# Kernel optimization log

Measured on AMD Instinct MI355X. Metric: run time of the kernel, lower is better.

Reference implementation:

```python
import jax, jax.numpy as jnp
import numpy as np
from jax import lax

B, T, V, LAT, U, P = 256, 128, 42, 200, 512, 3  # batch, seq, vocab, latent, lstm units, num_prop


def setup_inputs() -> dict:
    key = jax.random.key(0)
    ks = jax.random.split(key, 40)
    g = lambda i, shape, s=0.05: (jax.random.normal(ks[i], shape, jnp.float32) * s)
    inp = {
        'X': jax.random.randint(ks[0], (B, T), 0, V, jnp.int64 if jax.config.jax_enable_x64 else jnp.int32),
        'Y': jax.random.randint(ks[1], (B, T), 0, V, jnp.int32),
        'C': jax.random.normal(ks[2], (B, P), jnp.float32),
        'L': jax.random.randint(ks[3], (B,), 1, T + 1, jnp.int32),
        'eps': jax.random.normal(ks[4], (B, LAT), jnp.float32),
        'emb_enc': g(5, (V, LAT), 0.1),
        'emb_dec': g(6, (V, LAT), 0.1),
        # encoder stacked LSTM: layer0 input dim = LAT + P, layers 1-2 input dim = U
        'enc_k0': g(7, (LAT + P, 4 * U)), 'enc_rk0': g(8, (U, 4 * U)), 'enc_b0': jnp.zeros((4 * U,), jnp.float32),
        'enc_k1': g(9, (U, 4 * U)), 'enc_rk1': g(10, (U, 4 * U)), 'enc_b1': jnp.zeros((4 * U,), jnp.float32),
        'enc_k2': g(11, (U, 4 * U)), 'enc_rk2': g(12, (U, 4 * U)), 'enc_b2': jnp.zeros((4 * U,), jnp.float32),
        # decoder stacked LSTM: layer0 input dim = 2*LAT + P
        'dec_k0': g(13, (2 * LAT + P, 4 * U)), 'dec_rk0': g(14, (U, 4 * U)), 'dec_b0': jnp.zeros((4 * U,), jnp.float32),
        'dec_k1': g(15, (U, 4 * U)), 'dec_rk1': g(16, (U, 4 * U)), 'dec_b1': jnp.zeros((4 * U,), jnp.float32),
        'dec_k2': g(17, (U, 4 * U)), 'dec_rk2': g(18, (U, 4 * U)), 'dec_b2': jnp.zeros((4 * U,), jnp.float32),
        'Wm': g(19, (U, LAT)), 'bm': jnp.zeros((LAT,), jnp.float32),
        'Ws': g(20, (U, LAT)), 'bs': jnp.zeros((LAT,), jnp.float32),
        'Wo': g(21, (U, V)), 'bo': jnp.zeros((V,), jnp.float32),
    }
    return inp


def _lstm_step(x, h, c, k, rk, b):
    # Keras LSTMCell gate order: i, f, g(candidate), o
    z = x @ k + h @ rk + b
    i, f, gg, o = jnp.split(z, 4, axis=-1)
    c2 = jax.nn.sigmoid(f) * c + jax.nn.sigmoid(i) * jnp.tanh(gg)
    h2 = jax.nn.sigmoid(o) * jnp.tanh(c2)
    return h2, c2


def _run_stacked(inp, params):
    # inp: [B, T, D]; params: list of 3 (kernel, recurrent_kernel, bias)
    b = inp.shape[0]
    init = tuple((jnp.zeros((b, U), inp.dtype), jnp.zeros((b, U), inp.dtype)) for _ in range(3))

    def scan_fn(carry, x_t):
        h_in = x_t
        new = []
        for (h, c), (k, rk, bb) in zip(carry, params):
            h2, c2 = _lstm_step(h_in, h, c, k, rk, bb)
            new.append((h2, c2))
            h_in = h2
        return tuple(new), h_in

    carry, ys = lax.scan(scan_fn, init, jnp.swapaxes(inp, 0, 1))
    return jnp.swapaxes(ys, 0, 1), carry  # [B,T,U], final states


def reference(X, Y, C, L, eps, emb_enc, emb_dec,
              enc_k0, enc_rk0, enc_b0, enc_k1, enc_rk1, enc_b1, enc_k2, enc_rk2, enc_b2,
              dec_k0, dec_rk0, dec_b0, dec_k1, dec_rk1, dec_b1, dec_k2, dec_rk2, dec_b2,
              Wm, bm, Ws, bs, Wo, bo):
    enc_params = [(enc_k0, enc_rk0, enc_b0), (enc_k1, enc_rk1, enc_b1), (enc_k2, enc_rk2, enc_b2)]
    dec_params = [(dec_k0, dec_rk0, dec_b0), (dec_k1, dec_rk1, dec_b1), (dec_k2, dec_rk2, dec_b2)]

    # ---- encode ----
    Xe = emb_enc[X]                                       # [B,T,LAT]
    Ct = jnp.broadcast_to(C[:, None, :], (B, T, P))
    enc_in = jnp.concatenate([Xe, Ct], axis=-1)           # [B,T,LAT+P]
    _, enc_states = _run_stacked(enc_in, enc_params)
    h = enc_states[-1][1]                                 # CELL state of last layer (state[-1][1])
    mean = h @ Wm + bm
    log_sigma = h @ Ws + bs
    z = mean + jnp.exp(log_sigma / 2.0) * eps             # [B,LAT]

    # ---- decode ----
    Zt = jnp.broadcast_to(z[:, None, :], (B, T, LAT))
    Xd = emb_dec[X]
    dec_in = jnp.concatenate([Zt, Xd, Ct], axis=-1)       # [B,T,2*LAT+P]
    dec_out, _ = _run_stacked(dec_in, dec_params)
    pre = dec_out @ Wo + bo                               # pre-softmax logits [B,T,V]

    # ---- losses ----
    logp = jax.nn.log_softmax(pre, axis=-1)
    ce = -jnp.take_along_axis(logp, Y[..., None].astype(jnp.int32), axis=-1)[..., 0]  # [B,T]
    weights = (jnp.arange(T)[None, :] < L[:, None]).astype(jnp.float32)
    recon = jnp.mean(ce * weights)
    latent = -0.5 * jnp.mean(1.0 + log_sigma - jnp.square(mean) - jnp.exp(log_sigma))
    loss = recon + latent
    return loss, recon, latent
```

## Files before the change

### kernel.cpp

```cpp
#include <hip/hip_runtime.h>

#define B_ 256
#define T_ 128
#define V_ 42
#define LAT_ 200
#define U_ 512
#define G4_ 2048
#define NBLK 196
#define FI(r, m) ((((r) * 2) + (m)) * 32)
#define SLOT_ ((size_t)B_ * U_)
#define LS_ ((size_t)129 * SLOT_)

typedef unsigned short ushort_t;
typedef __attribute__((ext_vector_type(8))) short bf8;
typedef __attribute__((ext_vector_type(4))) float f4;

__device__ __forceinline__ ushort_t f2bf(float f) {
  union { float f; unsigned int i; } v; v.f = f;
  unsigned int r = v.i + 0x7fffu + ((v.i >> 16) & 1u);
  return (ushort_t)(r >> 16);
}
__device__ __forceinline__ float sigf(float x) { return 1.f / (1.f + __expf(-x)); }
__device__ __forceinline__ float tanhfast(float x) {
  float e = __expf(2.f * x);
  return 1.f - 2.f / (e + 1.f);
}
__device__ __forceinline__ void wait_vm0() {
  asm volatile("s_waitcnt vmcnt(0)" ::: "memory");
}
__device__ __forceinline__ void st_wt_b16(void* p, ushort_t v) {
  unsigned int vv = v;
  asm volatile("global_store_short %0, %1, off sc0 sc1" :: "v"(p), "v"(vv) : "memory");
}
__device__ __forceinline__ void st_wt_b32(void* p, unsigned int v) {
  asm volatile("global_store_dword %0, %1, off sc0 sc1" :: "v"(p), "v"(v) : "memory");
}

__global__ __launch_bounds__(256) void table_kernel(const float* emb, const float* k0, int roff, float* table) {
  int v = blockIdx.x, tid = threadIdx.x;
  __shared__ float e[LAT_];
  for (int i = tid; i < LAT_; i += 256) e[i] = emb[v * LAT_ + i];
  __syncthreads();
  for (int j = tid; j < G4_; j += 256) {
    float s = 0.f;
    for (int n = 0; n < LAT_; n++) s += e[n] * k0[(size_t)(roff + n) * G4_ + j];
    table[v * G4_ + j] = s;
  }
}

__device__ __forceinline__ size_t mat_off_u4(int m) {
  if (m == 0) return 0;
  if (m == 1) return 147456;
  if (m < 10) return 360448 + (size_t)(m - 2) * 131072;
  return 1409024;
}

struct SwzSrc {
  const float *enc_rk0, *enc_k0, *enc_b0;
  const float *dec_rk0, *dec_k0, *dec_b0;
  const float *tabE, *tabD;
  const float *encK1, *encR1, *encK2, *encR2;
  const float *decK1, *decR1, *decK2, *decR2;
  const float *Wo;
  ushort_t* dst;
};

__device__ float swz_val(const SwzSrc& s, int mat, int k, int n) {
  switch (mat) {
    case 0: {
      if (k < 512) return s.enc_rk0[(size_t)k * G4_ + n];
      int i = k - 512;
      if (i < 42) return s.tabE[(size_t)i * G4_ + n];
      if (i < 45) return s.enc_k0[(size_t)(200 + i - 42) * G4_ + n];
      if (i == 45) return s.enc_b0[n];
      return 0.f;
    }
    case 1: {
      if (k < 512) return s.dec_rk0[(size_t)k * G4_ + n];
      int i = k - 512;
      if (i < 200) return s.dec_k0[(size_t)i * G4_ + n];
      if (i < 256) return 0.f;
      i -= 256;
      if (i < 42) return s.tabD[(size_t)i * G4_ + n];
      if (i < 45) return s.dec_k0[(size_t)(400 + i - 42) * G4_ + n];
      if (i == 45) return s.dec_b0[n];
      return 0.f;
    }
    case 2: return s.encK1[(size_t)k * G4_ + n];
    case 3: return s.encR1[(size_t)k * G4_ + n];
    case 4: return s.encK2[(size_t)k * G4_ + n];
    case 5: return s.encR2[(size_t)k * G4_ + n];
    case 6: return s.decK1[(size_t)k * G4_ + n];
    case 7: return s.decR1[(size_t)k * G4_ + n];
    case 8: return s.decK2[(size_t)k * G4_ + n];
    case 9: return s.decR2[(size_t)k * G4_ + n];
    default: return (n < V_) ? s.Wo[(size_t)k * V_ + n] : 0.f;
  }
}

__global__ __launch_bounds__(256) void swz_ext_kernel(SwzSrc s) {
  int b = blockIdx.x, tid = threadIdx.x;
  int mat, nt16;
  if (b < 1280) { mat = b >> 7; nt16 = b & 127; } else { mat = 10; nt16 = b - 1280; }
  int ktMax = (mat == 0) ? 18 : (mat == 1) ? 26 : 16;
  int lane = tid & 63, l15 = lane & 15, q = lane >> 4;
  int n = nt16 * 16 + l15;
  uint4* dst = (uint4*)s.dst;
  size_t off = mat_off_u4(mat);
  for (int kt = tid >> 6; kt < ktMax; kt += 4) {
    ushort_t o[8];
    int kb = kt * 32 + q * 8;
#pragma unroll
    for (int j = 0; j < 8; j++) o[j] = f2bf(swz_val(s, mat, kb + j, n));
    dst[off + ((size_t)nt16 * ktMax + kt) * 64 + lane] = *(const uint4*)o;
  }
}

struct PP {
  const ushort_t* swz;
  ushort_t* ring;
  float* c2g; ushort_t* zf16; float* sums; int* bar; int* gen; int* flg; float* out;
  const float *enc_b1, *enc_b2, *dec_b1, *dec_b2;
  const float *Wm, *bm, *Ws, *bs, *eps, *C, *bo;
  const int *X, *Y, *Lb;
};

__device__ __forceinline__ void grid_barrier(int* bar, int* gen) {
  __builtin_amdgcn_fence(__ATOMIC_RELEASE, "agent");
  __syncthreads();
  if (threadIdx.x == 0) {
    int g = __hip_atomic_load(gen, __ATOMIC_RELAXED, __HIP_MEMORY_SCOPE_AGENT);
    if (__hip_atomic_fetch_add(bar, 1, __ATOMIC_ACQ_REL, __HIP_MEMORY_SCOPE_AGENT) == NBLK - 1) {
      __hip_atomic_store(bar, 0, __ATOMIC_RELAXED, __HIP_MEMORY_SCOPE_AGENT);
      __hip_atomic_store(gen, g + 1, __ATOMIC_RELEASE, __HIP_MEMORY_SCOPE_AGENT);
    } else {
      int gg;
      do {
        __builtin_amdgcn_s_sleep(8);
        gg = __hip_atomic_load(gen, __ATOMIC_ACQUIRE, __HIP_MEMORY_SCOPE_AGENT);
      } while (gg == g);
    }
  }
  __syncthreads();
  __builtin_amdgcn_fence(__ATOMIC_ACQUIRE, "agent");
}

__device__ __forceinline__ void wait_flags(const int* f, int cnt, int target) {
  int lane = threadIdx.x & 63;
  bool need = (lane * 2) < cnt;
  const unsigned long long* a = (const unsigned long long*)f + (need ? lane : 0);
  for (;;) {
    unsigned long long v = __hip_atomic_load(a, __ATOMIC_RELAXED, __HIP_MEMORY_SCOPE_AGENT);
    bool bad = need && ((int)v < target || (int)(v >> 32) < target);
    if (__ballot(bad) == 0ull) return;
    __builtin_amdgcn_s_sleep(8);
  }
}

#define MFMA(a, bfrag, c) __builtin_amdgcn_mfma_f32_16x16x32_bf16((a), (bfrag), (c), 0, 0, 0)

__global__ __launch_bounds__(256, 1) void persist(PP p) {
  __shared__ uint4 wlds4[8192];
  const int b = blockIdx.x, tid = threadIdx.x;
  const int lane = tid & 63, w = tid >> 6, q = lane >> 4, l15 = lane & 15;
  const int role = b < 64 ? 0 : b < 128 ? 1 : b < 192 ? 2 : 3;
  const int idx = b & 63;
  const int ut = idx >> 1;
  const int mi = idx & 1;
  const int m0 = mi * 128;
  const int rw = m0 + w * 32;
  const int u = ut * 16 + l15;
  const uint4* swzU4 = (const uint4*)p.swz;
  const int cb = b - 192;

  unsigned char* tok = (unsigned char*)wlds4 + 106496;
  unsigned char* ytok = (unsigned char*)wlds4 + 49152;

  ushort_t cb0[2][3];
  if (role == 0) {
#pragma unroll
    for (int ms = 0; ms < 2; ms++)
#pragma unroll
      for (int j = 0; j < 3; j++) cb0[ms][j] = f2bf(p.C[(rw + ms * 16 + l15) * 3 + j]);
  }

  const int pubidx = FI(role, mi) + ut;

  float ce_local = 0.f;
  float boR0 = 0.f, boR1 = 0.f, boR2 = 0.f;
  int Lr[4] = {0, 0, 0, 0};
  int pub = 0;

  for (int phase = 0; phase < 2; phase++) {
    const bool dec = (phase == 1);

    if (dec) {
      grid_barrier(p.bar, p.gen);
      if (b < 50) {
        int lat0 = b * 4;
        int row = tid;
        float m[4], ls[4];
#pragma unroll
        for (int lc = 0; lc < 4; lc++) { m[lc] = p.bm[lat0 + lc]; ls[lc] = p.bs[lat0 + lc]; }
        const float* cr = p.c2g + (size_t)row * U_;
        for (int k = 0; k < U_; k++) {
          float hv = cr[k];
#pragma unroll
          for (int lc = 0; lc < 4; lc++) {
            m[lc] += hv * p.Wm[k * LAT_ + lat0 + lc];
            ls[lc] += hv * p.Ws[k * LAT_ + lat0 + lc];
          }
        }
        float kl = 0.f;
#pragma unroll
        for (int lc = 0; lc < 4; lc++) {
          int lat = lat0 + lc;
          float zz = m[lc] + __expf(0.5f * ls[lc]) * p.eps[row * LAT_ + lat];
          p.zf16[row * 256 + lat] = f2bf(zz);
          kl += 1.f + ls[lc] - m[lc] * m[lc] - __expf(ls[lc]);
        }
        float* red = (float*)wlds4;
        red[tid] = kl; __syncthreads();
        for (int st = 128; st > 0; st >>= 1) { if (tid < st) red[tid] += red[tid + st]; __syncthreads(); }
        if (tid == 0) atomicAdd(p.sums + 1, red[0]);
      }
      __syncthreads();
    }

    if (role == 0) {
      if (!dec) {
        size_t mo = mat_off_u4(0);
        for (int g = 0; g < 4; g++) {
          int nt16 = g * 32 + ut;
          size_t src = mo + (size_t)nt16 * 18 * 64;
          int dst = g * 18 * 64;
          for (int i = tid; i < 18 * 64; i += 256) wlds4[dst + i] = swzU4[src + i];
        }
        for (int i = tid; i < 128 * T_; i += 256) {
          int r = i >> 7, t = i & 127;
          tok[r * 133 + t] = (unsigned char)p.X[(size_t)(m0 + r) * T_ + t];
        }
      } else {
        size_t mo = mat_off_u4(1);
        for (int g = 0; g < 4; g++) {
          int nt16 = g * 32 + ut;
          size_t src = mo + (size_t)nt16 * 26 * 64;
          int dst = g * 18 * 64;
          for (int i = tid; i < 16 * 64; i += 256) wlds4[dst + i] = swzU4[src + i];
          for (int i = tid; i < 2 * 64; i += 256) wlds4[dst + 16 * 64 + i] = swzU4[src + 24 * 64 + i];
          for (int i = tid; i < 8 * 64; i += 256) wlds4[4608 + g * 512 + i] = swzU4[src + 16 * 64 + i];
        }
      }
    } else if (role <= 2) {
      int matK = dec ? (role == 1 ? 6 : 8) : (role == 1 ? 2 : 4);
      for (int gm = 0; gm < 2; gm++) {
        size_t mo = mat_off_u4(matK + gm);
        for (int g = 0; g < 4; g++) {
          int nt16 = g * 32 + ut;
          size_t src = mo + (size_t)nt16 * 1024;
          int dst = gm * 4096 + g * 1024;
          for (int i = tid; i < 1024; i += 256) wlds4[dst + i] = swzU4[src + i];
        }
      }
    } else if (dec) {
      size_t mo = mat_off_u4(10);
      for (int i = tid; i < 3072; i += 256) wlds4[i] = swzU4[mo + i];
      for (int i = tid; i < 64 * T_; i += 256) {
        int r = i >> 7, t = i & 127;
        ytok[r * 133 + t] = (unsigned char)p.Y[(size_t)(cb * 64 + r) * T_ + t];
      }
      int r0c = cb * 64 + w * 16;
      boR0 = p.bo[l15]; boR1 = p.bo[16 + l15]; boR2 = (l15 < 10) ? p.bo[32 + l15] : 0.f;
#pragma unroll
      for (int r = 0; r < 4; r++) Lr[r] = p.Lb[r0c + q * 4 + r];
    }
    __syncthreads();

    float creg[2][4];
#pragma unroll
    for (int ms = 0; ms < 2; ms++)
#pragma unroll
      for (int r = 0; r < 4; r++) creg[ms][r] = 0.f;
    float bias[4] = {0.f, 0.f, 0.f, 0.f};
    if (role == 1 || role == 2) {
      const float* bb = dec ? (role == 1 ? p.dec_b1 : p.dec_b2) : (role == 1 ? p.enc_b1 : p.enc_b2);
#pragma unroll
      for (int g = 0; g < 4; g++) bias[g] = bb[g * 512 + u];
    }

    const int* myp = nullptr; int myc = 0;
    if (role == 0) {
      if (w == 0) { myp = p.flg + FI(0, mi); myc = 32; }
    } else if (role == 1) {
      if (w == 0) { myp = p.flg + FI(0, mi); myc = 32; }
      else if (w == 1) { myp = p.flg + FI(1, mi); myc = 32; }
    } else if (role == 2) {
      if (w == 0) { myp = p.flg + FI(1, mi); myc = 32; }
      else if (w == 1) { myp = p.flg + FI(2, mi); myc = 32; }
    } else {
      if (w == 0 && dec) { myp = p.flg + FI(2, cb >> 1); myc = 32; }
    }

    grid_barrier(p.bar, p.gen);

    f4 zacc[2][4];
#pragma unroll
    for (int ms = 0; ms < 2; ms++)
#pragma unroll
      for (int g = 0; g < 4; g++) zacc[ms][g] = (f4){0.f, 0.f, 0.f, 0.f};
    if (role == 0 && dec) {
      const ushort_t* Az0 = p.zf16 + (rw + l15) * 256 + q * 8;
#pragma unroll
      for (int kz = 0; kz < 8; kz++) {
        bf8 a0 = *(const bf8*)(Az0 + kz * 32);
        bf8 a1 = *(const bf8*)(Az0 + 16 * 256 + kz * 32);
#pragma unroll
        for (int g = 0; g < 4; g++) {
          bf8 bbf = *(const bf8*)&wlds4[4608 + g * 512 + kz * 64 + lane];
          zacc[0][g] = MFMA(a0, bbf, zacc[0][g]);
          zacc[1][g] = MFMA(a1, bbf, zacc[1][g]);
        }
      }
    }

    const int smax = dec ? T_ + 3 : T_ + 2;
    for (int s = 0; s < smax; s++) {
      pub++;
      if (myc) wait_flags(myp, myc, pub - 1);
      __syncthreads();

      const int lag = (role <= 2) ? role : 3;
      const int t = s - lag;
      if (role == 3) {
        if (dec && t >= 0 && t < T_) {
          int r0c = cb * 64 + w * 16;
          const ushort_t* Ar = p.ring + 2 * LS_ + (size_t)(t + 1) * SLOT_ + (size_t)(r0c + l15) * U_ + q * 8;
          f4 a3[3];
#pragma unroll
          for (int nt = 0; nt < 3; nt++) a3[nt] = (f4){0.f, 0.f, 0.f, 0.f};
#pragma unroll 4
          for (int kt = 0; kt < 16; kt++) {
            bf8 a = *(const bf8*)(Ar + kt * 32);
#pragma unroll
            for (int nt = 0; nt < 3; nt++) {
              bf8 bbf = *(const bf8*)&wlds4[nt * 1024 + kt * 64 + lane];
              a3[nt] = MFMA(a, bbf, a3[nt]);
            }
          }
#pragma unroll
          for (int r = 0; r < 4; r++) {
            float v0 = a3[0][r] + boR0;
            float v1 = a3[1][r] + boR1;
            float v2 = (l15 < 10) ? a3[2][r] + boR2 : -3.0e38f;
            float mx = fmaxf(fmaxf(v0, v1), v2);
            mx = fmaxf(mx, __shfl_xor(mx, 1)); mx = fmaxf(mx, __shfl_xor(mx, 2));
            mx = fmaxf(mx, __shfl_xor(mx, 4)); mx = fmaxf(mx, __shfl_xor(mx, 8));
            float se = __expf(v0 - mx) + __expf(v1 - mx) + ((l15 < 10) ? __expf(v2 - mx) : 0.f);
            int yv = ytok[(w * 16 + q * 4 + r) * 133 + t];
            float py = (l15 == yv ? v0 : 0.f) + (l15 + 16 == yv ? v1 : 0.f) + (l15 + 32 == yv ? v2 : 0.f);
            se += __shfl_xor(se, 1); se += __shfl_xor(se, 2); se += __shfl_xor(se, 4); se += __shfl_xor(se, 8);
            py += __shfl_xor(py, 1); py += __shfl_xor(py, 2); py += __shfl_xor(py, 4); py += __shfl_xor(py, 8);
            if (l15 == 0 && t < Lr[r]) ce_local += mx + __logf(se) - py;
          }
        }
      } else if (t >= 0 && t < T_) {
        f4 acc[2][4];
#pragma unroll
        for (int ms = 0; ms < 2; ms++)
#pragma unroll
          for (int g = 0; g < 4; g++) acc[ms][g] = zacc[ms][g];

        const ushort_t* hin = p.ring + (size_t)role * LS_ + (size_t)t * SLOT_;
        ushort_t* hout = p.ring + (size_t)role * LS_ + (size_t)(t + 1) * SLOT_;
        const ushort_t* Ah0 = hin + (size_t)(rw + l15) * U_ + q * 8;
        const ushort_t* Ah1 = Ah0 + 16 * U_;

        if (role == 0) {
          const int KT64 = 18 * 64;
#pragma unroll 4
          for (int kt = 0; kt < 16; kt++) {
            bf8 a0 = *(const bf8*)(Ah0 + kt * 32);
            bf8 a1 = *(const bf8*)(Ah1 + kt * 32);
#pragma unroll
            for (int g = 0; g < 4; g++) {
              bf8 bbf = *(const bf8*)&wlds4[g * KT64 + kt * 64 + lane];
              acc[0][g] = MFMA(a0, bbf, acc[0][g]);
              acc[1][g] = MFMA(a1, bbf, acc[1][g]);
            }
          }
          int xv0 = tok[(w * 32 + l15) * 133 + t];
          int xv1 = tok[(w * 32 + 16 + l15) * 133 + t];
#pragma unroll
          for (int ktc = 0; ktc < 2; ktc++) {
            union { ushort_t us[8]; bf8 v; } a0u, a1u;
#pragma unroll
            for (int j = 0; j < 8; j++) {
              int id = ktc * 32 + q * 8 + j;
              ushort_t v0 = (id == xv0) ? (ushort_t)0x3F80 : (ushort_t)0;
              ushort_t v1 = (id == xv1) ? (ushort_t)0x3F80 : (ushort_t)0;
              if (id >= 42 && id < 45) { v0 = cb0[0][id - 42]; v1 = cb0[1][id - 42]; }
              if (id == 45) { v0 = 0x3F80; v1 = 0x3F80; }
              a0u.us[j] = v0; a1u.us[j] = v1;
            }
            int kt = 16 + ktc;
#pragma unroll
            for (int g = 0; g < 4; g++) {
              bf8 bbf = *(const bf8*)&wlds4[g * KT64 + kt * 64 + lane];
              acc[0][g] = MFMA(a0u.v, bbf, acc[0][g]);
              acc[1][g] = MFMA(a1u.v, bbf, acc[1][g]);
            }
          }
        } else {
          const ushort_t* xin = p.ring + (size_t)(role - 1) * LS_ + (size_t)(t + 1) * SLOT_;
          const ushort_t* Ax0 = xin + (size_t)(rw + l15) * U_ + q * 8;
          const ushort_t* Ax1 = Ax0 + 16 * U_;
#pragma unroll 4
          for (int kt = 0; kt < 16; kt++) {
            bf8 a0 = *(const bf8*)(Ax0 + kt * 32);
            bf8 a1 = *(const bf8*)(Ax1 + kt * 32);
#pragma unroll
            for (int g = 0; g < 4; g++) {
              bf8 bbf = *(const bf8*)&wlds4[g * 1024 + kt * 64 + lane];
              acc[0][g] = MFMA(a0, bbf, acc[0][g]);
              acc[1][g] = MFMA(a1, bbf, acc[1][g]);
            }
          }
#pragma unroll 4
          for (int kt = 0; kt < 16; kt++) {
            bf8 a0 = *(const bf8*)(Ah0 + kt * 32);
            bf8 a1 = *(const bf8*)(Ah1 + kt * 32);
#pragma unroll
            for (int g = 0; g < 4; g++) {
              bf8 bbf = *(const bf8*)&wlds4[4096 + g * 1024 + kt * 64 + lane];
              acc[0][g] = MFMA(a0, bbf, acc[0][g]);
              acc[1][g] = MFMA(a1, bbf, acc[1][g]);
            }
          }
        }

#pragma unroll
        for (int ms = 0; ms < 2; ms++)
#pragma unroll
          for (int r = 0; r < 4; r++) {
            int row = rw + ms * 16 + q * 4 + r;
            float zi = acc[ms][0][r] + bias[0];
            float zf = acc[ms][1][r] + bias[1];
            float zg = acc[ms][2][r] + bias[2];
            float zo = acc[ms][3][r] + bias[3];
            float cp = creg[ms][r];
            float cn = sigf(zf) * cp + sigf(zi) * tanhfast(zg);
            float hn = sigf(zo) * tanhfast(cn);
            creg[ms][r] = cn;
            st_wt_b16(&hout[(size_t)row * U_ + u], f2bf(hn));
            if (!dec && role == 2 && t == T_ - 1) p.c2g[(size_t)row * U_ + u] = cn;
          }
      }
      wait_vm0();
      __syncthreads();
      if (tid == 0 && role < 3) st_wt_b32(p.flg + pubidx, (unsigned int)pub);
    }
  }

  if (role == 3 && l15 == 0) atomicAdd(p.sums + 0, ce_local);
  grid_barrier(p.bar, p.gen);
  if (b == 0 && tid == 0) {
    float recon = p.sums[0] * (1.f / ((float)B_ * (float)T_));
    float latent = -0.5f * p.sums[1] * (1.f / ((float)B_ * (float)LAT_));
    p.out[0] = recon + latent;
    p.out[1] = recon;
    p.out[2] = latent;
  }
}

extern "C" void kernel_launch(void* const* d_in, const int* in_sizes, int n_in,
                              void* d_out, int out_size, void* d_ws, size_t ws_size,
                              hipStream_t stream) {
  const int*   X       = (const int*)d_in[0];
  const int*   Y       = (const int*)d_in[1];
  const float* C       = (const float*)d_in[2];
  const int*   L       = (const int*)d_in[3];
  const float* eps     = (const float*)d_in[4];
  const float* emb_enc = (const float*)d_in[5];
  const float* emb_dec = (const float*)d_in[6];
  const float* enc_k0  = (const float*)d_in[7];
  const float* enc_rk0 = (const float*)d_in[8];
  const float* enc_b0  = (const float*)d_in[9];
  const float* enc_k1  = (const float*)d_in[10];
  const float* enc_rk1 = (const float*)d_in[11];
  const float* enc_b1  = (const float*)d_in[12];
  const float* enc_k2  = (const float*)d_in[13];
  const float* enc_rk2 = (const float*)d_in[14];
  const float* enc_b2  = (const float*)d_in[15];
  const float* dec_k0  = (const float*)d_in[16];
  const float* dec_rk0 = (const float*)d_in[17];
  const float* dec_b0  = (const float*)d_in[18];
  const float* dec_k1  = (const float*)d_in[19];
  const float* dec_rk1 = (const float*)d_in[20];
  const float* dec_b1  = (const float*)d_in[21];
  const float* dec_k2  = (const float*)d_in[22];
  const float* dec_rk2 = (const float*)d_in[23];
  const float* dec_b2  = (const float*)d_in[24];
  const float* Wm      = (const float*)d_in[25];
  const float* bm      = (const float*)d_in[26];
  const float* Ws      = (const float*)d_in[27];
  const float* bs      = (const float*)d_in[28];
  const float* Wo      = (const float*)d_in[29];
  const float* bo      = (const float*)d_in[30];
  float* out = (float*)d_out;
  (void)in_sizes; (void)n_in; (void)out_size; (void)ws_size;

  char* wsb = (char*)d_ws;
  size_t o = 0;
  auto take = [&](size_t bytes) -> char* { char* p = wsb + o; o += (bytes + 255) & ~(size_t)255; return p; };

  float* c2g  = (float*)take((size_t)B_ * U_ * 4);
  ushort_t* zf16 = (ushort_t*)take((size_t)B_ * 256 * 2);
  float* sums = (float*)take(8);
  int* bar = (int*)take(4);
  int* gen = (int*)take(4);
  int* flg = (int*)take(4 * 2 * 32 * 4);
  size_t zero_bytes = o;
  ushort_t* ring = (ushort_t*)take(3 * LS_ * 2);
  ushort_t* swz = (ushort_t*)take((size_t)1412096 * 16);
  float* tabE = (float*)take((size_t)V_ * G4_ * 4);
  float* tabD = (float*)take((size_t)V_ * G4_ * 4);

  hipMemsetAsync(wsb, 0, zero_bytes, stream);
  for (int l = 0; l < 3; l++)
    hipMemsetAsync(ring + (size_t)l * LS_, 0, SLOT_ * 2, stream);

  table_kernel<<<V_, 256, 0, stream>>>(emb_enc, enc_k0, 0, tabE);
  table_kernel<<<V_, 256, 0, stream>>>(emb_dec, dec_k0, 200, tabD);

  SwzSrc ss;
  ss.enc_rk0 = enc_rk0; ss.enc_k0 = enc_k0; ss.enc_b0 = enc_b0;
  ss.dec_rk0 = dec_rk0; ss.dec_k0 = dec_k0; ss.dec_b0 = dec_b0;
  ss.tabE = tabE; ss.tabD = tabD;
  ss.encK1 = enc_k1; ss.encR1 = enc_rk1; ss.encK2 = enc_k2; ss.encR2 = enc_rk2;
  ss.decK1 = dec_k1; ss.decR1 = dec_rk1; ss.decK2 = dec_k2; ss.decR2 = dec_rk2;
  ss.Wo = Wo; ss.dst = swz;
  swz_ext_kernel<<<1283, 256, 0, stream>>>(ss);

  PP pp;
  pp.swz = swz; pp.ring = ring;
  pp.c2g = c2g; pp.zf16 = zf16; pp.sums = sums; pp.bar = bar; pp.gen = gen; pp.flg = flg; pp.out = out;
  pp.enc_b1 = enc_b1; pp.enc_b2 = enc_b2; pp.dec_b1 = dec_b1; pp.dec_b2 = dec_b2;
  pp.Wm = Wm; pp.bm = bm; pp.Ws = Ws; pp.bs = bs; pp.eps = eps; pp.C = C; pp.bo = bo;
  pp.X = X; pp.Y = Y; pp.Lb = L;
  persist<<<NBLK, 256, 0, stream>>>(pp);
}
```

Baseline: 5.388 ms.

## Interleave block roles across XCDs, grow grid to 256, and tighten spin-waits

Block roles are now assigned by blockIdx modulo 8, so each LSTM layer/half and the output blocks are spread across XCDs. The grid grows to 256 blocks, and the extra blocks act as helpers that only do the latent projection and skip the recurrent loop. The grid barrier sleeps less between polls, and the flag wait polls one int per lane with no sleep, to cut wake-up latency on each per-step handoff. The h-state store now does a plain store followed by a write-through store, which adds a redundant write, and the busier polling adds memory traffic.

```diff
diff --git a/kernel.cpp b/kernel.cpp
--- a/kernel.cpp
+++ b/kernel.cpp
@@ -6,7 +6,7 @@
 #define LAT_ 200
 #define U_ 512
 #define G4_ 2048
-#define NBLK 196
+#define NBLK 256
 #define FI(r, m) ((((r) * 2) + (m)) * 32)
 #define SLOT_ ((size_t)B_ * U_)
 #define LS_ ((size_t)129 * SLOT_)
@@ -136,7 +136,7 @@
     } else {
       int gg;
       do {
-        __builtin_amdgcn_s_sleep(8);
+        __builtin_amdgcn_s_sleep(1);
         gg = __hip_atomic_load(gen, __ATOMIC_ACQUIRE, __HIP_MEMORY_SCOPE_AGENT);
       } while (gg == g);
     }
@@ -147,14 +147,12 @@
 
 __device__ __forceinline__ void wait_flags(const int* f, int cnt, int target) {
   int lane = threadIdx.x & 63;
-  bool need = (lane * 2) < cnt;
-  const unsigned long long* a = (const unsigned long long*)f + (need ? lane : 0);
-  for (;;) {
-    unsigned long long v = __hip_atomic_load(a, __ATOMIC_RELAXED, __HIP_MEMORY_SCOPE_AGENT);
-    bool bad = need && ((int)v < target || (int)(v >> 32) < target);
-    if (__ballot(bad) == 0ull) return;
-    __builtin_amdgcn_s_sleep(8);
-  }
+  const int* a = f + (lane < cnt ? lane : 0);
+  bool bad;
+  do {
+    int v = __hip_atomic_load(a, __ATOMIC_RELAXED, __HIP_MEMORY_SCOPE_AGENT);
+    bad = (lane < cnt) && (v < target);
+  } while (__ballot(bad) != 0ull);
 }
 
 #define MFMA(a, bfrag, c) __builtin_amdgcn_mfma_f32_16x16x32_bf16((a), (bfrag), (c), 0, 0, 0)
@@ -163,15 +161,17 @@
   __shared__ uint4 wlds4[8192];
   const int b = blockIdx.x, tid = threadIdx.x;
   const int lane = tid & 63, w = tid >> 6, q = lane >> 4, l15 = lane & 15;
-  const int role = b < 64 ? 0 : b < 128 ? 1 : b < 192 ? 2 : 3;
-  const int idx = b & 63;
-  const int ut = idx >> 1;
-  const int mi = idx & 1;
+
+  const int grp = b & 7, rank = b >> 3;
+  int role, mi = 0, cb = 0, pid = -1;
+  if (grp < 6) { role = grp >> 1; mi = grp & 1; }
+  else if (grp == 6 && rank < 4) { role = 3; cb = rank; mi = rank >> 1; }
+  else { role = 4; pid = (grp == 6) ? rank - 4 : 28 + rank; }
+  const int ut = rank;
   const int m0 = mi * 128;
   const int rw = m0 + w * 32;
   const int u = ut * 16 + l15;
   const uint4* swzU4 = (const uint4*)p.swz;
-  const int cb = b - 192;
 
   unsigned char* tok = (unsigned char*)wlds4 + 106496;
   unsigned char* ytok = (unsigned char*)wlds4 + 49152;
@@ -196,8 +196,8 @@
 
     if (dec) {
       grid_barrier(p.bar, p.gen);
-      if (b < 50) {
-        int lat0 = b * 4;
+      if (pid >= 0 && pid < 50) {
+        int lat0 = pid * 4;
         int row = tid;
         float m[4], ls[4];
 #pragma unroll
@@ -262,7 +262,7 @@
           for (int i = tid; i < 1024; i += 256) wlds4[dst + i] = swzU4[src + i];
         }
       }
-    } else if (dec) {
+    } else if (role == 3 && dec) {
       size_t mo = mat_off_u4(10);
       for (int i = tid; i < 3072; i += 256) wlds4[i] = swzU4[mo + i];
       for (int i = tid; i < 64 * T_; i += 256) {
@@ -297,7 +297,7 @@
     } else if (role == 2) {
       if (w == 0) { myp = p.flg + FI(1, mi); myc = 32; }
       else if (w == 1) { myp = p.flg + FI(2, mi); myc = 32; }
-    } else {
+    } else if (role == 3) {
       if (w == 0 && dec) { myp = p.flg + FI(2, cb >> 1); myc = 32; }
     }
 
@@ -323,141 +323,146 @@
       }
     }
 
-    const int smax = dec ? T_ + 3 : T_ + 2;
-    for (int s = 0; s < smax; s++) {
-      pub++;
-      if (myc) wait_flags(myp, myc, pub - 1);
-      __syncthreads();
-
-      const int lag = (role <= 2) ? role : 3;
-      const int t = s - lag;
-      if (role == 3) {
-        if (dec && t >= 0 && t < T_) {
-          int r0c = cb * 64 + w * 16;
-          const ushort_t* Ar = p.ring + 2 * LS_ + (size_t)(t + 1) * SLOT_ + (size_t)(r0c + l15) * U_ + q * 8;
-          f4 a3[3];
-#pragma unroll
-          for (int nt = 0; nt < 3; nt++) a3[nt] = (f4){0.f, 0.f, 0.f, 0.f};
+    if (role <= 3) {
+      const int smax = dec ? T_ + 3 : T_ + 2;
+      for (int s = 0; s < smax; s++) {
+        pub++;
+        if (myc) wait_flags(myp, myc, pub - 1);
+        __syncthreads();
+
+        const int lag = (role <= 2) ? role : 3;
+        const int t = s - lag;
+        if (role == 3) {
+          if (dec && t >= 0 && t < T_) {
+            int r0c = cb * 64 + w * 16;
+            const ushort_t* Ar = p.ring + 2 * LS_ + (size_t)(t + 1) * SLOT_ + (size_t)(r0c + l15) * U_ + q * 8;
+            f4 a3[3];
+#pragma unroll
+            for (int nt = 0; nt < 3; nt++) a3[nt] = (f4){0.f, 0.f, 0.f, 0.f};
 #pragma unroll 4
-          for (int kt = 0; kt < 16; kt++) {
-            bf8 a = *(const bf8*)(Ar + kt * 32);
-#pragma unroll
-            for (int nt = 0; nt < 3; nt++) {
-              bf8 bbf = *(const bf8*)&wlds4[nt * 1024 + kt * 64 + lane];
-              a3[nt] = MFMA(a, bbf, a3[nt]);
+            for (int kt = 0; kt < 16; kt++) {
+              bf8 a = *(const bf8*)(Ar + kt * 32);
+#pragma unroll
+              for (int nt = 0; nt < 3; nt++) {
+                bf8 bbf = *(const bf8*)&wlds4[nt * 1024 + kt * 64 + lane];
+                a3[nt] = MFMA(a, bbf, a3[nt]);
+              }
+            }
+#pragma unroll
+            for (int r = 0; r < 4; r++) {
+              float v0 = a3[0][r] + boR0;
+              float v1 = a3[1][r] + boR1;
+              float v2 = (l15 < 10) ? a3[2][r] + boR2 : -3.0e38f;
+              float mx = fmaxf(fmaxf(v0, v1), v2);
+              mx = fmaxf(mx, __shfl_xor(mx, 1)); mx = fmaxf(mx, __shfl_xor(mx, 2));
+              mx = fmaxf(mx, __shfl_xor(mx, 4)); mx = fmaxf(mx, __shfl_xor(mx, 8));
+              float se = __expf(v0 - mx) + __expf(v1 - mx) + ((l15 < 10) ? __expf(v2 - mx) : 0.f);
+              int yv = ytok[(w * 16 + q * 4 + r) * 133 + t];
+              float py = (l15 == yv ? v0 : 0.f) + (l15 + 16 == yv ? v1 : 0.f) + (l15 + 32 == yv ? v2 : 0.f);
+              se += __shfl_xor(se, 1); se += __shfl_xor(se, 2); se += __shfl_xor(se, 4); se += __shfl_xor(se, 8);
+              py += __shfl_xor(py, 1); py += __shfl_xor(py, 2); py += __shfl_xor(py, 4); py += __shfl_xor(py, 8);
+              if (l15 == 0 && t < Lr[r]) ce_local += mx + __logf(se) - py;
             }
           }
-#pragma unroll
-          for (int r = 0; r < 4; r++) {
-            float v0 = a3[0][r] + boR0;
-            float v1 = a3[1][r] + boR1;
-            float v2 = (l15 < 10) ? a3[2][r] + boR2 : -3.0e38f;
-            float mx = fmaxf(fmaxf(v0, v1), v2);
-            mx = fmaxf(mx, __shfl_xor(mx, 1)); mx = fmaxf(mx, __shfl_xor(mx, 2));
-            mx = fmaxf(mx, __shfl_xor(mx, 4)); mx = fmaxf(mx, __shfl_xor(mx, 8));
-            float se = __expf(v0 - mx) + __expf(v1 - mx) + ((l15 < 10) ? __expf(v2 - mx) : 0.f);
-            int yv = ytok[(w * 16 + q * 4 + r) * 133 + t];
-            float py = (l15 == yv ? v0 : 0.f) + (l15 + 16 == yv ? v1 : 0.f) + (l15 + 32 == yv ? v2 : 0.f);
-            se += __shfl_xor(se, 1); se += __shfl_xor(se, 2); se += __shfl_xor(se, 4); se += __shfl_xor(se, 8);
-            py += __shfl_xor(py, 1); py += __shfl_xor(py, 2); py += __shfl_xor(py, 4); py += __shfl_xor(py, 8);
-            if (l15 == 0 && t < Lr[r]) ce_local += mx + __logf(se) - py;
+        } else if (t >= 0 && t < T_) {
+          f4 acc[2][4];
+#pragma unroll
+          for (int ms = 0; ms < 2; ms++)
+#pragma unroll
+            for (int g = 0; g < 4; g++) acc[ms][g] = zacc[ms][g];
+
+          const ushort_t* hin = p.ring + (size_t)role * LS_ + (size_t)t * SLOT_;
+          ushort_t* hout = p.ring + (size_t)role * LS_ + (size_t)(t + 1) * SLOT_;
+          const ushort_t* Ah0 = hin + (size_t)(rw + l15) * U_ + q * 8;
+          const ushort_t* Ah1 = Ah0 + 16 * U_;
+
+          if (role == 0) {
+            const int KT64 = 18 * 64;
+#pragma unroll 4
+            for (int kt = 0; kt < 16; kt++) {
+              bf8 a0 = *(const bf8*)(Ah0 + kt * 32);
+              bf8 a1 = *(const bf8*)(Ah1 + kt * 32);
+#pragma unroll
+              for (int g = 0; g < 4; g++) {
+                bf8 bbf = *(const bf8*)&wlds4[g * KT64 + kt * 64 + lane];
+                acc[0][g] = MFMA(a0, bbf, acc[0][g]);
+                acc[1][g] = MFMA(a1, bbf, acc[1][g]);
+              }
+            }
+            int xv0 = tok[(w * 32 + l15) * 133 + t];
+            int xv1 = tok[(w * 32 + 16 + l15) * 133 + t];
+#pragma unroll
+            for (int ktc = 0; ktc < 2; ktc++) {
+              union { ushort_t us[8]; bf8 v; } a0u, a1u;
+#pragma unroll
+              for (int j = 0; j < 8; j++) {
+                int id = ktc * 32 + q * 8 + j;
+                ushort_t v0 = (id == xv0) ? (ushort_t)0x3F80 : (ushort_t)0;
+                ushort_t v1 = (id == xv1) ? (ushort_t)0x3F80 : (ushort_t)0;
+                if (id >= 42 && id < 45) { v0 = cb0[0][id - 42]; v1 = cb0[1][id - 42]; }
+                if (id == 45) { v0 = 0x3F80; v1 = 0x3F80; }
+                a0u.us[j] = v0; a1u.us[j] = v1;
+              }
+              int kt = 16 + ktc;
+#pragma unroll
+              for (int g = 0; g < 4; g++) {
+                bf8 bbf = *(const bf8*)&wlds4[g * KT64 + kt * 64 + lane];
+                acc[0][g] = MFMA(a0u.v, bbf, acc[0][g]);
+                acc[1][g] = MFMA(a1u.v, bbf, acc[1][g]);
+              }
+            }
+          } else {
+            const ushort_t* xin = p.ring + (size_t)(role - 1) * LS_ + (size_t)(t + 1) * SLOT_;
+            const ushort_t* Ax0 = xin + (size_t)(rw + l15) * U_ + q * 8;
+            const ushort_t* Ax1 = Ax0 + 16 * U_;
+#pragma unroll 4
+            for (int kt = 0; kt < 16; kt++) {
+              bf8 a0 = *(const bf8*)(Ax0 + kt * 32);
+              bf8 a1 = *(const bf8*)(Ax1 + kt * 32);
+#pragma unroll
+              for (int g = 0; g < 4; g++) {
+                bf8 bbf = *(const bf8*)&wlds4[g * 1024 + kt * 64 + lane];
+                acc[0][g] = MFMA(a0, bbf, acc[0][g]);
+                acc[1][g] = MFMA(a1, bbf, acc[1][g]);
+              }
+            }
+#pragma unroll 4
+            for (int kt = 0; kt < 16; kt++) {
+              bf8 a0 = *(const bf8*)(Ah0 + kt * 32);
+              bf8 a1 = *(const bf8*)(Ah1 + kt * 32);
+#pragma unroll
+              for (int g = 0; g < 4; g++) {
+                bf8 bbf = *(const bf8*)&wlds4[4096 + g * 1024 + kt * 64 + lane];
+                acc[0][g] = MFMA(a0, bbf, acc[0][g]);
+                acc[1][g] = MFMA(a1, bbf, acc[1][g]);
+              }
+            }
           }
-        }
-      } else if (t >= 0 && t < T_) {
-        f4 acc[2][4];
-#pragma unroll
-        for (int ms = 0; ms < 2; ms++)
-#pragma unroll
-          for (int g = 0; g < 4; g++) acc[ms][g] = zacc[ms][g];
-
-        const ushort_t* hin = p.ring + (size_t)role * LS_ + (size_t)t * SLOT_;
-        ushort_t* hout = p.ring + (size_t)role * LS_ + (size_t)(t + 1) * SLOT_;
-        const ushort_t* Ah0 = hin + (size_t)(rw + l15) * U_ + q * 8;
-        const ushort_t* Ah1 = Ah0 + 16 * U_;
-
-        if (role == 0) {
-          const int KT64 = 18 * 64;
-#pragma unroll 4
-          for (int kt = 0; kt < 16; kt++) {
-            bf8 a0 = *(const bf8*)(Ah0 + kt * 32);
-            bf8 a1 = *(const bf8*)(Ah1 + kt * 32);
-#pragma unroll
-            for (int g = 0; g < 4; g++) {
-              bf8 bbf = *(const bf8*)&wlds4[g * KT64 + kt * 64 + lane];
-              acc[0][g] = MFMA(a0, bbf, acc[0][g]);
-              acc[1][g] = MFMA(a1, bbf, acc[1][g]);
-            }
-          }
-          int xv0 = tok[(w * 32 + l15) * 133 + t];
-          int xv1 = tok[(w * 32 + 16 + l15) * 133 + t];
-#pragma unroll
-          for (int ktc = 0; ktc < 2; ktc++) {
-            union { ushort_t us[8]; bf8 v; } a0u, a1u;
-#pragma unroll
-            for (int j = 0; j < 8; j++) {
-              int id = ktc * 32 + q * 8 + j;
-              ushort_t v0 = (id == xv0) ? (ushort_t)0x3F80 : (ushort_t)0;
-              ushort_t v1 = (id == xv1) ? (ushort_t)0x3F80 : (ushort_t)0;
-              if (id >= 42 && id < 45) { v0 = cb0[0][id - 42]; v1 = cb0[1][id - 42]; }
-              if (id == 45) { v0 = 0x3F80; v1 = 0x3F80; }
-              a0u.us[j] = v0; a1u.us[j] = v1;
-            }
-            int kt = 16 + ktc;
-#pragma unroll
-            for (int g = 0; g < 4; g++) {
-              bf8 bbf = *(const bf8*)&wlds4[g * KT64 + kt * 64 + lane];
-              acc[0][g] = MFMA(a0u.v, bbf, acc[0][g]);
-              acc[1][g] = MFMA(a1u.v, bbf, acc[1][g]);
-            }
-          }
-        } else {
-          const ushort_t* xin = p.ring + (size_t)(role - 1) * LS_ + (size_t)(t + 1) * SLOT_;
-          const ushort_t* Ax0 = xin + (size_t)(rw + l15) * U_ + q * 8;
-          const ushort_t* Ax1 = Ax0 + 16 * U_;
-#pragma unroll 4
-          for (int kt = 0; kt < 16; kt++) {
-            bf8 a0 = *(const bf8*)(Ax0 + kt * 32);
-            bf8 a1 = *(const bf8*)(Ax1 + kt * 32);
-#pragma unroll
-            for (int g = 0; g < 4; g++) {
-              bf8 bbf = *(const bf8*)&wlds4[g * 1024 + kt * 64 + lane];
-              acc[0][g] = MFMA(a0, bbf, acc[0][g]);
-              acc[1][g] = MFMA(a1, bbf, acc[1][g]);
-            }
-          }
-#pragma unroll 4
-          for (int kt = 0; kt < 16; kt++) {
-            bf8 a0 = *(const bf8*)(Ah0 + kt * 32);
-            bf8 a1 = *(const bf8*)(Ah1 + kt * 32);
-#pragma unroll
-            for (int g = 0; g < 4; g++) {
-              bf8 bbf = *(const bf8*)&wlds4[4096 + g * 1024 + kt * 64 + lane];
-              acc[0][g] = MFMA(a0, bbf, acc[0][g]);
-              acc[1][g] = MFMA(a1, bbf, acc[1][g]);
-            }
-          }
-        }
-
-#pragma unroll
-        for (int ms = 0; ms < 2; ms++)
-#pragma unroll
-          for (int r = 0; r < 4; r++) {
-            int row = rw + ms * 16 + q * 4 + r;
-            float zi = acc[ms][0][r] + bias[0];
-            float zf = acc[ms][1][r] + bias[1];
-            float zg = acc[ms][2][r] + bias[2];
-            float zo = acc[ms][3][r] + bias[3];
-            float cp = creg[ms][r];
-            float cn = sigf(zf) * cp + sigf(zi) * tanhfast(zg);
-            float hn = sigf(zo) * tanhfast(cn);
-            creg[ms][r] = cn;
-            st_wt_b16(&hout[(size_t)row * U_ + u], f2bf(hn));
-            if (!dec && role == 2 && t == T_ - 1) p.c2g[(size_t)row * U_ + u] = cn;
-          }
+
+#pragma unroll
+          for (int ms = 0; ms < 2; ms++)
+#pragma unroll
+            for (int r = 0; r < 4; r++) {
+              int row = rw + ms * 16 + q * 4 + r;
+              float zi = acc[ms][0][r] + bias[0];
+              float zf = acc[ms][1][r] + bias[1];
+              float zg = acc[ms][2][r] + bias[2];
+              float zo = acc[ms][3][r] + bias[3];
+              float cp = creg[ms][r];
+              float cn = sigf(zf) * cp + sigf(zi) * tanhfast(zg);
+              float hn = sigf(zo) * tanhfast(cn);
+              creg[ms][r] = cn;
+              ushort_t hv = f2bf(hn);
+              ushort_t* addr = &hout[(size_t)row * U_ + u];
+              *addr = hv;
+              st_wt_b16(addr, hv);
+              if (!dec && role == 2 && t == T_ - 1) p.c2g[(size_t)row * U_ + u] = cn;
+            }
+        }
+        wait_vm0();
+        __syncthreads();
+        if (tid == 0 && role < 3) st_wt_b32(p.flg + pubidx, (unsigned int)pub);
       }
-      wait_vm0();
-      __syncthreads();
-      if (tid == 0 && role < 3) st_wt_b32(p.flg + pubidx, (unsigned int)pub);
     }
   }
 
```

Result: slower. 9.032 ms (+67.6%).
